# Performance work log

Hardware: AMD Instinct MI355X
Metric: run time of the kernel (lower is better)

The kernel has to match this reference:

```python
import jax, jax.numpy as jnp
import numpy as np

BN_EPS = 1e-4  # matches torch.nn.BatchNorm1d(eps=0.0001)

def setup_inputs() -> dict:
    key = jax.random.key(0)
    ks = jax.random.split(key, 8)
    N, T, D_in, D_out = 512, 64, 1024, 1024
    return {
        "input_feature_st": jax.random.randint(ks[0], (N, T, D_in), 0, 2).astype(jnp.float32),
        "input_features_sc": jax.random.normal(ks[1], (N, D_in), dtype=jnp.float32),
        "weight": jax.random.normal(ks[2], (D_out, D_in), dtype=jnp.float32) * 0.03,
        "bias": jax.random.normal(ks[3], (D_out,), dtype=jnp.float32) * 0.1,
        "gamma": jax.random.normal(ks[4], (D_out,), dtype=jnp.float32) * 2.0,  # nn.init.normal_(bn.weight, 0, 2.0)
        "beta": jnp.zeros((D_out,), dtype=jnp.float32),
        "running_mean": jax.random.normal(ks[5], (D_out,), dtype=jnp.float32) * 0.1,
        "running_var": jax.random.uniform(ks[6], (D_out,), dtype=jnp.float32, minval=0.5, maxval=1.5),
    }

def _if_scan(pot_in, bias_step):
    # pot_in: (N, T, D_out); bias_step: (D_out,) -> spikes (N, T, D_out)
    pot0 = jnp.zeros(pot_in.shape[::2], dtype=pot_in.dtype)  # (N, D_out)
    def step(pot, p_t):
        pot = pot + p_t + bias_step
        spk = (pot >= 1.0).astype(pot.dtype)
        return pot - spk, spk
    _, spikes_t = jax.lax.scan(step, pot0, jnp.swapaxes(pot_in, 0, 1))  # (T, N, D)
    return jnp.swapaxes(spikes_t, 0, 1)

def reference(input_feature_st, input_features_sc, weight, bias, gamma, beta, running_mean, running_var):
    T = input_feature_st.shape[1]
    # ANN path: Linear + BN (eval stats) + ReLU
    lin = input_features_sc @ weight.T + bias                      # (N, D_out)
    out_bn = gamma * (lin - running_mean) / jnp.sqrt(running_var + BN_EPS) + beta
    ann_output = jax.nn.relu(out_bn)
    # Fold BN into weights for the SNN path (note: no eps, as in source)
    ratio = gamma / jnp.sqrt(running_var)
    w_norm = weight * ratio[:, None]                               # (D_out, D_in)
    b_norm = (bias - running_mean) * ratio + beta                  # (D_out,)
    # Integrate-and-fire scan over T
    pot_in = jnp.einsum("ntd,od->nto", input_feature_st, w_norm)  # (N, T, D_out)
    spike_out = _if_scan(pot_in, b_norm / T)
    spike_count_out = jnp.sum(spike_out, axis=1)                   # (N, D_out)
    return spike_out, spike_count_out
```

## Files before the change

### kernel.cpp

```cpp
#include <hip/hip_runtime.h>
#include <hip/hip_bf16.h>

typedef float  float4v __attribute__((ext_vector_type(4)));
typedef short  short8v __attribute__((ext_vector_type(8)));
typedef short  short4v __attribute__((ext_vector_type(4)));
typedef __bf16 bf16x8  __attribute__((ext_vector_type(8)));
typedef float  f32x4   __attribute__((ext_vector_type(4)));

constexpr int NB = 512, T = 64, DIN = 1024, DOUT = 1024;
constexpr int BM = 128, BN = 128, BK = 64;

constexpr size_t ABF_BYTES = (size_t)NB * T * DIN * 2;
constexpr size_t WN_BYTES  = (size_t)DOUT * DIN * 2;
constexpr size_t WS_BF16   = ABF_BYTES + WN_BYTES;

__device__ __forceinline__ short f2bf_rne(float x) {
    return __builtin_bit_cast(short, __float2bfloat16(x));
}
__device__ __forceinline__ short f2bf_trunc(float x) {
    return (short)(__builtin_bit_cast(unsigned int, x) >> 16);
}
__device__ __forceinline__ void load_lds_16B(const void* g, void* l) {
    __builtin_amdgcn_global_load_lds(
        (const __attribute__((address_space(1))) unsigned int*)g,
        (__attribute__((address_space(3))) unsigned int*)l, 16, 0, 0);
}

__global__ void __launch_bounds__(256)
prep_a_kernel(const float* __restrict__ A, short* __restrict__ Abf) {
    int idx = blockIdx.x * 256 + threadIdx.x;
    const float4v* p = (const float4v*)A + (size_t)idx * 2;
    float4v v0 = __builtin_nontemporal_load(p);
    float4v v1 = __builtin_nontemporal_load(p + 1);
    short8v s;
    #pragma unroll
    for (int j = 0; j < 4; j++) {
        s[j]     = f2bf_trunc(v0[j]);
        s[j + 4] = f2bf_trunc(v1[j]);
    }
    *((short8v*)Abf + idx) = s;
}

__global__ void __launch_bounds__(256)
fold_w_kernel(const float* __restrict__ W, const float* __restrict__ gamma,
              const float* __restrict__ rvar, short* __restrict__ Wn) {
    int idx = blockIdx.x * 256 + threadIdx.x;
    int o = idx >> 8;
    float r = gamma[o] / sqrtf(rvar[o]);
    float4v w = ((const float4v*)W)[idx];
    short4v s;
    #pragma unroll
    for (int j = 0; j < 4; j++) s[j] = f2bf_rne(w[j] * r);
    ((short4v*)Wn)[idx] = s;
}

__global__ void __launch_bounds__(256, 4)
snn_gemm_if_dma(const short* __restrict__ Abf,
                const short* __restrict__ Wn,
                const float* __restrict__ bias, const float* __restrict__ gamma,
                const float* __restrict__ beta, const float* __restrict__ rmean,
                const float* __restrict__ rvar, float* __restrict__ out) {
    __shared__ __align__(16) char smem[32768];
    __shared__ float bstepS[BN];
    char* AsS   = smem;
    char* BsS   = smem + 16384;
    float* potS = (float*)smem;

    const int tid = threadIdx.x;
    const int bs  = blockIdx.x;
    const int oB  = blockIdx.y * BN;

    if (tid < BN) {
        int o = oB + tid;
        float r = gamma[o] / sqrtf(rvar[o]);
        bstepS[tid] = ((bias[o] - rmean[o]) * r + beta[o]) * (1.0f / 64.0f);
    }

    const int lane = tid & 63;
    const int wv   = tid >> 6;
    const int wr   = wv & 1;
    const int wc   = wv >> 1;
    const int l15  = lane & 15;
    const int quad = lane >> 4;

    int srcOff[4];
    #pragma unroll
    for (int i = 0; i < 4; i++) {
        int s   = i * 256 + tid;
        int row = s >> 3;
        int ck  = (s & 7) ^ (row & 7);
        srcOff[i] = (row * DIN + ck * 8) * 2;
    }
    int aOff[4][2], bOff[4][2];
    #pragma unroll
    for (int i = 0; i < 4; i++) {
        int ra = wr * 64 + i * 16 + l15;
        int rb = wc * 64 + i * 16 + l15;
        #pragma unroll
        for (int ks = 0; ks < 2; ks++) {
            int c = ks * 4 + quad;
            aOff[i][ks] = (ra * 8 + (c ^ (ra & 7))) * 16;
            bOff[i][ks] = (rb * 8 + (c ^ (rb & 7))) * 16;
        }
    }

    f32x4 acc[4][4] = {};
    const char* Ab = (const char*)(Abf + (size_t)bs * BM * DIN);
    const char* Bb = (const char*)(Wn + (size_t)oB * DIN);

    for (int kb = 0; kb < DIN; kb += BK) {
        __syncthreads();
        const int kbB = kb * 2;
        #pragma unroll
        for (int i = 0; i < 4; i++) {
            int s = i * 256 + tid;
            load_lds_16B(Ab + srcOff[i] + kbB, AsS + s * 16);
            load_lds_16B(Bb + srcOff[i] + kbB, BsS + s * 16);
        }
        __syncthreads();

        #pragma unroll
        for (int ks = 0; ks < 2; ks++) {
            bf16x8 af[4], bf[4];
            #pragma unroll
            for (int i = 0; i < 4; i++)
                af[i] = __builtin_bit_cast(bf16x8, *(const short8v*)(AsS + aOff[i][ks]));
            #pragma unroll
            for (int i = 0; i < 4; i++)
                bf[i] = __builtin_bit_cast(bf16x8, *(const short8v*)(BsS + bOff[i][ks]));
            #pragma unroll
            for (int mi = 0; mi < 4; mi++)
                #pragma unroll
                for (int ni = 0; ni < 4; ni++)
                    acc[mi][ni] = __builtin_amdgcn_mfma_f32_16x16x32_bf16(
                        af[mi], bf[ni], acc[mi][ni], 0, 0, 0);
        }
    }

    __syncthreads();

    #pragma unroll 1
    for (int s = 0; s < 2; s++) {
        if (wr == s) {
            #pragma unroll
            for (int mi = 0; mi < 4; mi++)
                #pragma unroll
                for (int ni = 0; ni < 4; ni++)
                    #pragma unroll
                    for (int r = 0; r < 4; r++) {
                        int row = mi * 16 + quad * 4 + r;
                        int col = (wc * 64 + ni * 16 + l15) ^ (quad << 3);
                        potS[row * BN + col] = acc[mi][ni][r];
                    }
        }
        __syncthreads();
        if (tid < BN) {
            int n = bs * 2 + s;
            float pot = 0.f, cnt = 0.f;
            const float bst = bstepS[tid];
            float* so = out + (size_t)n * T * DOUT + oB + tid;
            for (int t = 0; t < T; t++) {
                pot += potS[t * BN + (tid ^ (((t >> 2) & 3) << 3))] + bst;
                float spk = (pot >= 1.0f) ? 1.0f : 0.0f;
                pot -= spk;
                cnt += spk;
                __builtin_nontemporal_store(spk, so + (size_t)t * DOUT);
            }
            __builtin_nontemporal_store(
                cnt, out + (size_t)NB * T * DOUT + (size_t)n * DOUT + oB + tid);
        }
        __syncthreads();
    }
}


constexpr int LDA_F = 72;
constexpr int A_BYTES_F = BM * LDA_F * 2;
constexpr int SMEM_F = A_BYTES_F + BN * BK * 2;

template <bool PREFOLD>
__global__ void __launch_bounds__(256)
snn_gemm_if(const float* __restrict__ A, const float* __restrict__ W,
            const short* __restrict__ Wn,
            const float* __restrict__ bias, const float* __restrict__ gamma,
            const float* __restrict__ beta, const float* __restrict__ rmean,
            const float* __restrict__ rvar, float* __restrict__ out) {
    __shared__ __align__(16) char smem[SMEM_F];
    __shared__ float ratioS[BN];
    __shared__ float bstepS[BN];
    short* AsS  = (short*)smem;
    short* BsS  = (short*)(smem + A_BYTES_F);
    float* potS = (float*)smem;

    const int tid   = threadIdx.x;
    const int by    = blockIdx.y;
    const int oBase = blockIdx.x * BN;

    if (tid < BN) {
        int o = oBase + tid;
        float r = gamma[o] / sqrtf(rvar[o]);
        ratioS[tid] = r;
        bstepS[tid] = ((bias[o] - rmean[o]) * r + beta[o]) * (1.0f / 64.0f);
    }
    __syncthreads();

    const int lane = tid & 63;
    const int wv   = tid >> 6;
    const int wr   = wv & 1;
    const int wc   = wv >> 1;
    const int l15  = lane & 15;
    const int quad = lane >> 4;

    f32x4 acc[4][4] = {};
    const float* Ab = A + (size_t)by * BM * DIN;

    for (int kb = 0; kb < DIN; kb += BK) {
        float4v av[4][2];
        #pragma unroll
        for (int i = 0; i < 4; i++) {
            int g = i * 256 + tid;
            int r = g >> 3, k8 = g & 7;
            const float4v* p = (const float4v*)(Ab + (size_t)r * DIN + kb + k8 * 8);
            av[i][0] = p[0];
            av[i][1] = p[1];
        }
        float4v bv[4][2];
        if constexpr (!PREFOLD) {
            #pragma unroll
            for (int i = 0; i < 4; i++) {
                int slot = i * 256 + tid;
                int r = slot >> 3, k8 = (slot & 7) ^ (r & 7);
                const float4v* p = (const float4v*)(W + (size_t)(oBase + r) * DIN + kb + k8 * 8);
                bv[i][0] = p[0];
                bv[i][1] = p[1];
            }
        }
        __syncthreads();

        if constexpr (PREFOLD) {
            #pragma unroll
            for (int i = 0; i < 4; i++) {
                int slot = i * 256 + tid;
                int r = slot >> 3, k8 = (slot & 7) ^ (r & 7);
                load_lds_16B(Wn + (size_t)(oBase + r) * DIN + kb + k8 * 8,
                             BsS + (size_t)slot * 8);
            }
        } else {
            #pragma unroll
            for (int i = 0; i < 4; i++) {
                int slot = i * 256 + tid;
                int r = slot >> 3;
                float rt = ratioS[r];
                short8v s;
                #pragma unroll
                for (int j = 0; j < 4; j++) {
                    s[j]     = f2bf_rne(bv[i][0][j] * rt);
                    s[j + 4] = f2bf_rne(bv[i][1][j] * rt);
                }
                *(short8v*)(BsS + (size_t)slot * 8) = s;
            }
        }
        #pragma unroll
        for (int i = 0; i < 4; i++) {
            int g = i * 256 + tid;
            int r = g >> 3, k8 = g & 7;
            short8v s;
            #pragma unroll
            for (int j = 0; j < 4; j++) {
                s[j]     = f2bf_trunc(av[i][0][j]);
                s[j + 4] = f2bf_trunc(av[i][1][j]);
            }
            *(short8v*)(&AsS[r * LDA_F + k8 * 8]) = s;
        }
        __syncthreads();

        #pragma unroll
        for (int ks = 0; ks < 2; ks++) {
            bf16x8 af[4], bfv[4];
            #pragma unroll
            for (int mi = 0; mi < 4; mi++)
                af[mi] = __builtin_bit_cast(bf16x8,
                    *(const short8v*)(&AsS[(wr * 64 + mi * 16 + l15) * LDA_F + ks * 32 + quad * 8]));
            #pragma unroll
            for (int ni = 0; ni < 4; ni++) {
                int row  = wc * 64 + ni * 16 + l15;
                int slot = row * 8 + ((ks * 4 + quad) ^ (l15 & 7));
                bfv[ni] = __builtin_bit_cast(bf16x8, *(const short8v*)(BsS + (size_t)slot * 8));
            }
            #pragma unroll
            for (int mi = 0; mi < 4; mi++)
                #pragma unroll
                for (int ni = 0; ni < 4; ni++)
                    acc[mi][ni] = __builtin_amdgcn_mfma_f32_16x16x32_bf16(
                        af[mi], bfv[ni], acc[mi][ni], 0, 0, 0);
        }
    }

    __syncthreads();

    #pragma unroll 1
    for (int s = 0; s < 2; s++) {
        if (wr == s) {
            #pragma unroll
            for (int mi = 0; mi < 4; mi++)
                #pragma unroll
                for (int ni = 0; ni < 4; ni++)
                    #pragma unroll
                    for (int r = 0; r < 4; r++)
                        potS[(mi * 16 + quad * 4 + r) * BN + wc * 64 + ni * 16 + l15] =
                            acc[mi][ni][r];
        }
        __syncthreads();
        if (tid < BN) {
            int n = by * 2 + s;
            float pot = 0.f, cnt = 0.f;
            const float bst = bstepS[tid];
            float* so = out + (size_t)n * T * DOUT + oBase + tid;
            for (int t = 0; t < T; t++) {
                pot += potS[t * BN + tid] + bst;
                float spk = (pot >= 1.0f) ? 1.0f : 0.0f;
                pot -= spk;
                cnt += spk;
                so[(size_t)t * DOUT] = spk;
            }
            out[(size_t)NB * T * DOUT + (size_t)n * DOUT + oBase + tid] = cnt;
        }
        __syncthreads();
    }
}

extern "C" void kernel_launch(void* const* d_in, const int* in_sizes, int n_in,
                              void* d_out, int out_size, void* d_ws, size_t ws_size,
                              hipStream_t stream) {
    const float* A     = (const float*)d_in[0];
    const float* W     = (const float*)d_in[2];
    const float* bias  = (const float*)d_in[3];
    const float* gamma = (const float*)d_in[4];
    const float* beta  = (const float*)d_in[5];
    const float* rmean = (const float*)d_in[6];
    const float* rvar  = (const float*)d_in[7];
    float* out = (float*)d_out;

    if (d_ws != nullptr && ws_size >= WS_BF16) {
        short* Abf = (short*)d_ws;
        short* Wn  = (short*)((char*)d_ws + ABF_BYTES);
        prep_a_kernel<<<(NB * T * DIN) / 8 / 256, 256, 0, stream>>>(A, Abf);
        fold_w_kernel<<<DOUT * DIN / 4 / 256, 256, 0, stream>>>(W, gamma, rvar, Wn);
        dim3 grid(NB / 2, DOUT / BN);
        snn_gemm_if_dma<<<grid, 256, 0, stream>>>(Abf, Wn, bias, gamma, beta,
                                                  rmean, rvar, out);
    } else if (d_ws != nullptr && ws_size >= WN_BYTES) {
        short* Wn = (short*)d_ws;
        fold_w_kernel<<<DOUT * DIN / 4 / 256, 256, 0, stream>>>(W, gamma, rvar, Wn);
        dim3 grid(DOUT / BN, NB / 2);
        snn_gemm_if<true><<<grid, 256, 0, stream>>>(A, W, Wn, bias, gamma, beta,
                                                    rmean, rvar, out);
    } else {
        dim3 grid(DOUT / BN, NB / 2);
        snn_gemm_if<false><<<grid, 256, 0, stream>>>(A, W, nullptr, bias, gamma, beta,
                                                     rmean, rvar, out);
    }
}
```

Measured before the change: 305.3 us.

## Use 256x256 tiles with triple-buffered async LDS pipeline and fused prep kernel

Replaces the 128x128 single-buffered bf16 GEMM with a 512-thread 256x256 tile kernel. It uses BK=32, three LDS buffers loaded by direct global-to-LDS DMA, and waits on vmcnt so loads overlap MFMA compute, with priority raised around the MFMA block. The two prep kernels for A conversion and W folding are merged into one launch. The larger tiles reduce global reloads of A and W, but the grid shrinks to 512 blocks, more LDS is used per block, and the scan epilogue now covers 4 batch rows per block.

```diff
diff --git a/kernel.cpp b/kernel.cpp
--- a/kernel.cpp
+++ b/kernel.cpp
@@ -8,7 +8,6 @@
 typedef float  f32x4   __attribute__((ext_vector_type(4)));
 
 constexpr int NB = 512, T = 64, DIN = 1024, DOUT = 1024;
-constexpr int BM = 128, BN = 128, BK = 64;
 
 constexpr size_t ABF_BYTES = (size_t)NB * T * DIN * 2;
 constexpr size_t WN_BYTES  = (size_t)DOUT * DIN * 2;
@@ -26,19 +25,36 @@
         (__attribute__((address_space(3))) unsigned int*)l, 16, 0, 0);
 }
 
+constexpr int PREP_A_BLOCKS = NB * T * DIN / 8 / 256;
+constexpr int PREP_W_BLOCKS = DOUT * DIN / 4 / 256;
+
 __global__ void __launch_bounds__(256)
-prep_a_kernel(const float* __restrict__ A, short* __restrict__ Abf) {
-    int idx = blockIdx.x * 256 + threadIdx.x;
-    const float4v* p = (const float4v*)A + (size_t)idx * 2;
-    float4v v0 = __builtin_nontemporal_load(p);
-    float4v v1 = __builtin_nontemporal_load(p + 1);
-    short8v s;
-    #pragma unroll
-    for (int j = 0; j < 4; j++) {
-        s[j]     = f2bf_trunc(v0[j]);
-        s[j + 4] = f2bf_trunc(v1[j]);
-    }
-    *((short8v*)Abf + idx) = s;
+prep_fused(const float* __restrict__ A, short* __restrict__ Abf,
+           const float* __restrict__ W, const float* __restrict__ gamma,
+           const float* __restrict__ rvar, short* __restrict__ Wn) {
+    const int b = blockIdx.x;
+    if (b < PREP_A_BLOCKS) {
+        int idx = b * 256 + threadIdx.x;
+        const float4v* p = (const float4v*)A + (size_t)idx * 2;
+        float4v v0 = __builtin_nontemporal_load(p);
+        float4v v1 = __builtin_nontemporal_load(p + 1);
+        short8v s;
+        #pragma unroll
+        for (int j = 0; j < 4; j++) {
+            s[j]     = f2bf_trunc(v0[j]);
+            s[j + 4] = f2bf_trunc(v1[j]);
+        }
+        *((short8v*)Abf + idx) = s;
+    } else {
+        int idx = (b - PREP_A_BLOCKS) * 256 + threadIdx.x;
+        int o = idx >> 8;
+        float r = gamma[o] / sqrtf(rvar[o]);
+        float4v w = ((const float4v*)W)[idx];
+        short4v s;
+        #pragma unroll
+        for (int j = 0; j < 4; j++) s[j] = f2bf_rne(w[j] * r);
+        ((short4v*)Wn)[idx] = s;
+    }
 }
 
 __global__ void __launch_bounds__(256)
@@ -54,23 +70,25 @@
     ((short4v*)Wn)[idx] = s;
 }
 
-__global__ void __launch_bounds__(256, 4)
-snn_gemm_if_dma(const short* __restrict__ Abf,
+constexpr int BM2 = 256, BN2 = 256, BK2 = 32;
+constexpr int NSTEP2 = DIN / BK2;
+constexpr int BUFB   = (BM2 + BN2) * BK2 * 2;
+constexpr int BREG   = BM2 * BK2 * 2;
+
+__global__ void __launch_bounds__(512, 2)
+snn_gemm_if_256(const short* __restrict__ Abf,
                 const short* __restrict__ Wn,
                 const float* __restrict__ bias, const float* __restrict__ gamma,
                 const float* __restrict__ beta, const float* __restrict__ rmean,
                 const float* __restrict__ rvar, float* __restrict__ out) {
-    __shared__ __align__(16) char smem[32768];
-    __shared__ float bstepS[BN];
-    char* AsS   = smem;
-    char* BsS   = smem + 16384;
-    float* potS = (float*)smem;
+    __shared__ __align__(16) char sm[3 * BUFB];
+    __shared__ float bstepS[BN2];
 
     const int tid = threadIdx.x;
-    const int bs  = blockIdx.x;
-    const int oB  = blockIdx.y * BN;
-
-    if (tid < BN) {
+    const int oB  = blockIdx.x * BN2;
+    const int bs  = blockIdx.y;
+
+    if (tid < BN2) {
         int o = oB + tid;
         float r = gamma[o] / sqrtf(rvar[o]);
         bstepS[tid] = ((bias[o] - rmean[o]) * r + beta[o]) * (1.0f / 64.0f);
@@ -78,89 +96,114 @@
 
     const int lane = tid & 63;
     const int wv   = tid >> 6;
-    const int wr   = wv & 1;
-    const int wc   = wv >> 1;
+    const int wr   = wv >> 2;
+    const int wc   = wv & 3;
     const int l15  = lane & 15;
     const int quad = lane >> 4;
 
-    int srcOff[4];
+    int aOff[8], bOff[4];
     #pragma unroll
-    for (int i = 0; i < 4; i++) {
-        int s   = i * 256 + tid;
-        int row = s >> 3;
-        int ck  = (s & 7) ^ (row & 7);
-        srcOff[i] = (row * DIN + ck * 8) * 2;
-    }
-    int aOff[4][2], bOff[4][2];
+    for (int mi = 0; mi < 8; mi++) {
+        int r = wr * 128 + mi * 16 + l15;
+        aOff[mi] = (r * 4 + (quad ^ ((r >> 1) & 3))) * 16;
+    }
     #pragma unroll
-    for (int i = 0; i < 4; i++) {
-        int ra = wr * 64 + i * 16 + l15;
-        int rb = wc * 64 + i * 16 + l15;
-        #pragma unroll
-        for (int ks = 0; ks < 2; ks++) {
-            int c = ks * 4 + quad;
-            aOff[i][ks] = (ra * 8 + (c ^ (ra & 7))) * 16;
-            bOff[i][ks] = (rb * 8 + (c ^ (rb & 7))) * 16;
-        }
-    }
-
-    f32x4 acc[4][4] = {};
-    const char* Ab = (const char*)(Abf + (size_t)bs * BM * DIN);
-    const char* Bb = (const char*)(Wn + (size_t)oB * DIN);
-
-    for (int kb = 0; kb < DIN; kb += BK) {
-        __syncthreads();
-        const int kbB = kb * 2;
-        #pragma unroll
-        for (int i = 0; i < 4; i++) {
-            int s = i * 256 + tid;
-            load_lds_16B(Ab + srcOff[i] + kbB, AsS + s * 16);
-            load_lds_16B(Bb + srcOff[i] + kbB, BsS + s * 16);
-        }
-        __syncthreads();
-
-        #pragma unroll
-        for (int ks = 0; ks < 2; ks++) {
-            bf16x8 af[4], bf[4];
-            #pragma unroll
-            for (int i = 0; i < 4; i++)
-                af[i] = __builtin_bit_cast(bf16x8, *(const short8v*)(AsS + aOff[i][ks]));
-            #pragma unroll
-            for (int i = 0; i < 4; i++)
-                bf[i] = __builtin_bit_cast(bf16x8, *(const short8v*)(BsS + bOff[i][ks]));
-            #pragma unroll
-            for (int mi = 0; mi < 4; mi++)
+    for (int ni = 0; ni < 4; ni++) {
+        int r = wc * 64 + ni * 16 + l15;
+        bOff[ni] = BREG + (r * 4 + (quad ^ ((r >> 1) & 3))) * 16;
+    }
+
+    f32x4 acc[8][4] = {};
+
+    const int s0 = tid, s1 = 512 + tid;
+    const int r0 = s0 >> 2, r1 = s1 >> 2;
+    const int c0 = (s0 & 3) ^ ((r0 >> 1) & 3);
+    const int c1 = (s1 & 3) ^ ((r1 >> 1) & 3);
+    const short* gA0 = Abf + (size_t)(bs * BM2 + r0) * DIN + c0 * 8;
+    const short* gA1 = Abf + (size_t)(bs * BM2 + r1) * DIN + c1 * 8;
+    const short* gB0 = Wn + (size_t)(oB + r0) * DIN + c0 * 8;
+    const short* gB1 = Wn + (size_t)(oB + r1) * DIN + c1 * 8;
+    const int dA0 = s0 * 16, dA1 = s1 * 16;
+    const int dB0 = BREG + s0 * 16, dB1 = BREG + s1 * 16;
+
+    auto STAGE = [&](int bufB) {
+        load_lds_16B(gA0, sm + bufB + dA0);
+        load_lds_16B(gA1, sm + bufB + dA1);
+        load_lds_16B(gB0, sm + bufB + dB0);
+        load_lds_16B(gB1, sm + bufB + dB1);
+        gA0 += BK2; gA1 += BK2; gB0 += BK2; gB1 += BK2;
+    };
+    auto COMPUTE = [&](int bufB) {
+        const char* base = sm + bufB;
+        bf16x8 af[8], bv[4];
+        #pragma unroll
+        for (int mi = 0; mi < 8; mi++)
+            af[mi] = __builtin_bit_cast(bf16x8, *(const short8v*)(base + aOff[mi]));
+        #pragma unroll
+        for (int ni = 0; ni < 4; ni++)
+            bv[ni] = __builtin_bit_cast(bf16x8, *(const short8v*)(base + bOff[ni]));
+        __builtin_amdgcn_s_setprio(1);
+        #pragma unroll
+        for (int mi = 0; mi < 8; mi++)
+            #pragma unroll
+            for (int ni = 0; ni < 4; ni++)
+                acc[mi][ni] = __builtin_amdgcn_mfma_f32_16x16x32_bf16(
+                    af[mi], bv[ni], acc[mi][ni], 0, 0, 0);
+        __builtin_amdgcn_s_setprio(0);
+    };
+
+    STAGE(0);
+    STAGE(BUFB);
+    asm volatile("s_waitcnt vmcnt(4)" ::: "memory");
+    __builtin_amdgcn_sched_barrier(0);
+    __builtin_amdgcn_s_barrier();
+    __builtin_amdgcn_sched_barrier(0);
+
+    int cb = 0, sb = 2 * BUFB;
+    #pragma unroll 1
+    for (int t = 0; t < NSTEP2 - 2; ++t) {
+        STAGE(sb);
+        COMPUTE(cb);
+        asm volatile("s_waitcnt vmcnt(4)" ::: "memory");
+        __builtin_amdgcn_sched_barrier(0);
+        __builtin_amdgcn_s_barrier();
+        __builtin_amdgcn_sched_barrier(0);
+        cb = (cb == 2 * BUFB) ? 0 : cb + BUFB;
+        sb = (sb == 2 * BUFB) ? 0 : sb + BUFB;
+    }
+    COMPUTE(0);
+    asm volatile("s_waitcnt vmcnt(0)" ::: "memory");
+    __builtin_amdgcn_sched_barrier(0);
+    __builtin_amdgcn_s_barrier();
+    __builtin_amdgcn_sched_barrier(0);
+    COMPUTE(BUFB);
+
+    __syncthreads();
+
+    float* potS = (float*)sm;
+    #pragma unroll
+    for (int s = 0; s < 4; ++s) {
+        if (wr == (s >> 1)) {
+            const int mib = (s & 1) * 4;
+            #pragma unroll
+            for (int m2 = 0; m2 < 4; ++m2)
                 #pragma unroll
-                for (int ni = 0; ni < 4; ni++)
-                    acc[mi][ni] = __builtin_amdgcn_mfma_f32_16x16x32_bf16(
-                        af[mi], bf[ni], acc[mi][ni], 0, 0, 0);
-        }
-    }
-
-    __syncthreads();
-
-    #pragma unroll 1
-    for (int s = 0; s < 2; s++) {
-        if (wr == s) {
-            #pragma unroll
-            for (int mi = 0; mi < 4; mi++)
-                #pragma unroll
-                for (int ni = 0; ni < 4; ni++)
+                for (int ni = 0; ni < 4; ++ni)
                     #pragma unroll
-                    for (int r = 0; r < 4; r++) {
-                        int row = mi * 16 + quad * 4 + r;
+                    for (int r = 0; r < 4; ++r) {
+                        int rl  = m2 * 16 + quad * 4 + r;
                         int col = (wc * 64 + ni * 16 + l15) ^ (quad << 3);
-                        potS[row * BN + col] = acc[mi][ni][r];
+                        potS[rl * BN2 + col] = acc[mib + m2][ni][r];
                     }
         }
         __syncthreads();
-        if (tid < BN) {
-            int n = bs * 2 + s;
+        if (tid < BN2) {
+            int n = bs * 4 + s;
             float pot = 0.f, cnt = 0.f;
             const float bst = bstepS[tid];
             float* so = out + (size_t)n * T * DOUT + oB + tid;
             for (int t = 0; t < T; t++) {
-                pot += potS[t * BN + (tid ^ (((t >> 2) & 3) << 3))] + bst;
+                pot += potS[t * BN2 + (tid ^ (((t >> 2) & 3) << 3))] + bst;
                 float spk = (pot >= 1.0f) ? 1.0f : 0.0f;
                 pot -= spk;
                 cnt += spk;
@@ -174,6 +217,7 @@
 }
 
 
+constexpr int BM = 128, BN = 128, BK = 64;
 constexpr int LDA_F = 72;
 constexpr int A_BYTES_F = BM * LDA_F * 2;
 constexpr int SMEM_F = A_BYTES_F + BN * BK * 2;
@@ -344,10 +388,10 @@
     if (d_ws != nullptr && ws_size >= WS_BF16) {
         short* Abf = (short*)d_ws;
         short* Wn  = (short*)((char*)d_ws + ABF_BYTES);
-        prep_a_kernel<<<(NB * T * DIN) / 8 / 256, 256, 0, stream>>>(A, Abf);
-        fold_w_kernel<<<DOUT * DIN / 4 / 256, 256, 0, stream>>>(W, gamma, rvar, Wn);
-        dim3 grid(NB / 2, DOUT / BN);
-        snn_gemm_if_dma<<<grid, 256, 0, stream>>>(Abf, Wn, bias, gamma, beta,
+        prep_fused<<<PREP_A_BLOCKS + PREP_W_BLOCKS, 256, 0, stream>>>(
+            A, Abf, W, gamma, rvar, Wn);
+        dim3 grid(DOUT / BN2, NB / 4);
+        snn_gemm_if_256<<<grid, 512, 0, stream>>>(Abf, Wn, bias, gamma, beta,
                                                   rmean, rvar, out);
     } else if (d_ws != nullptr && ws_size >= WN_BYTES) {
         short* Wn = (short*)d_ws;
```

Result: slower. 320.7 us (+5.0%).

## Double-buffer A tiles in LDS, load B fragments directly to registers, remap grid

Applied to the files above, without the earlier changes.

Restructures the GEMM main loop so A tiles are double-buffered in LDS via async global-to-LDS loads, which leaves one barrier per K step instead of two. B (the folded weights) is read straight from global memory into registers instead of being staged through LDS. The 1D grid is remapped so the 8 output-column tiles of the same row panel spread across XCDs, and the two prep kernels are fused into a single launch. The trade-off is more global traffic for B, which should mostly hit cache, plus higher register pressure, and launch bounds drop to 3 blocks per CU.

```diff
diff --git a/kernel.cpp b/kernel.cpp
--- a/kernel.cpp
+++ b/kernel.cpp
@@ -8,7 +8,6 @@
 typedef float  f32x4   __attribute__((ext_vector_type(4)));
 
 constexpr int NB = 512, T = 64, DIN = 1024, DOUT = 1024;
-constexpr int BM = 128, BN = 128, BK = 64;
 
 constexpr size_t ABF_BYTES = (size_t)NB * T * DIN * 2;
 constexpr size_t WN_BYTES  = (size_t)DOUT * DIN * 2;
@@ -26,19 +25,36 @@
         (__attribute__((address_space(3))) unsigned int*)l, 16, 0, 0);
 }
 
+constexpr int PREP_A_BLOCKS = NB * T * DIN / 8 / 256;
+constexpr int PREP_W_BLOCKS = DOUT * DIN / 4 / 256;
+
 __global__ void __launch_bounds__(256)
-prep_a_kernel(const float* __restrict__ A, short* __restrict__ Abf) {
-    int idx = blockIdx.x * 256 + threadIdx.x;
-    const float4v* p = (const float4v*)A + (size_t)idx * 2;
-    float4v v0 = __builtin_nontemporal_load(p);
-    float4v v1 = __builtin_nontemporal_load(p + 1);
-    short8v s;
-    #pragma unroll
-    for (int j = 0; j < 4; j++) {
-        s[j]     = f2bf_trunc(v0[j]);
-        s[j + 4] = f2bf_trunc(v1[j]);
-    }
-    *((short8v*)Abf + idx) = s;
+prep_fused(const float* __restrict__ A, short* __restrict__ Abf,
+           const float* __restrict__ W, const float* __restrict__ gamma,
+           const float* __restrict__ rvar, short* __restrict__ Wn) {
+    const int b = blockIdx.x;
+    if (b < PREP_A_BLOCKS) {
+        int idx = b * 256 + threadIdx.x;
+        const float4v* p = (const float4v*)A + (size_t)idx * 2;
+        float4v v0 = __builtin_nontemporal_load(p);
+        float4v v1 = __builtin_nontemporal_load(p + 1);
+        short8v s;
+        #pragma unroll
+        for (int j = 0; j < 4; j++) {
+            s[j]     = f2bf_trunc(v0[j]);
+            s[j + 4] = f2bf_trunc(v1[j]);
+        }
+        *((short8v*)Abf + idx) = s;
+    } else {
+        int idx = (b - PREP_A_BLOCKS) * 256 + threadIdx.x;
+        int o = idx >> 8;
+        float r = gamma[o] / sqrtf(rvar[o]);
+        float4v w = ((const float4v*)W)[idx];
+        short4v s;
+        #pragma unroll
+        for (int j = 0; j < 4; j++) s[j] = f2bf_rne(w[j] * r);
+        ((short4v*)Wn)[idx] = s;
+    }
 }
 
 __global__ void __launch_bounds__(256)
@@ -54,21 +70,24 @@
     ((short4v*)Wn)[idx] = s;
 }
 
-__global__ void __launch_bounds__(256, 4)
-snn_gemm_if_dma(const short* __restrict__ Abf,
-                const short* __restrict__ Wn,
-                const float* __restrict__ bias, const float* __restrict__ gamma,
-                const float* __restrict__ beta, const float* __restrict__ rmean,
-                const float* __restrict__ rvar, float* __restrict__ out) {
-    __shared__ __align__(16) char smem[32768];
+constexpr int BM = 128, BN = 128, BK = 64;
+constexpr int NT = DIN / BK;
+constexpr int ABUF = BM * BK * 2;
+
+__global__ void __launch_bounds__(256, 3)
+snn_gemm_if_breg(const short* __restrict__ Abf,
+                 const short* __restrict__ Wn,
+                 const float* __restrict__ bias, const float* __restrict__ gamma,
+                 const float* __restrict__ beta, const float* __restrict__ rmean,
+                 const float* __restrict__ rvar, float* __restrict__ out) {
+    __shared__ __align__(16) char sm[2 * ABUF];
     __shared__ float bstepS[BN];
-    char* AsS   = smem;
-    char* BsS   = smem + 16384;
-    float* potS = (float*)smem;
 
     const int tid = threadIdx.x;
-    const int bs  = blockIdx.x;
-    const int oB  = blockIdx.y * BN;
+    const int b     = blockIdx.x;
+    const int work  = (b & 7) * 256 + (b >> 3);
+    const int panel = work >> 3;
+    const int oB    = (work & 7) * BN;
 
     if (tid < BN) {
         int o = oB + tid;
@@ -91,54 +110,68 @@
         int ck  = (s & 7) ^ (row & 7);
         srcOff[i] = (row * DIN + ck * 8) * 2;
     }
-    int aOff[4][2], bOff[4][2];
+    int aOff[4][2];
     #pragma unroll
     for (int i = 0; i < 4; i++) {
         int ra = wr * 64 + i * 16 + l15;
-        int rb = wc * 64 + i * 16 + l15;
         #pragma unroll
         for (int ks = 0; ks < 2; ks++) {
             int c = ks * 4 + quad;
             aOff[i][ks] = (ra * 8 + (c ^ (ra & 7))) * 16;
-            bOff[i][ks] = (rb * 8 + (c ^ (rb & 7))) * 16;
-        }
-    }
+        }
+    }
+
+    const short* gBf[4];
+    #pragma unroll
+    for (int ni = 0; ni < 4; ni++)
+        gBf[ni] = Wn + (size_t)(oB + wc * 64 + ni * 16 + l15) * DIN + quad * 8;
 
     f32x4 acc[4][4] = {};
-    const char* Ab = (const char*)(Abf + (size_t)bs * BM * DIN);
-    const char* Bb = (const char*)(Wn + (size_t)oB * DIN);
-
-    for (int kb = 0; kb < DIN; kb += BK) {
-        __syncthreads();
-        const int kbB = kb * 2;
-        #pragma unroll
-        for (int i = 0; i < 4; i++) {
-            int s = i * 256 + tid;
-            load_lds_16B(Ab + srcOff[i] + kbB, AsS + s * 16);
-            load_lds_16B(Bb + srcOff[i] + kbB, BsS + s * 16);
-        }
-        __syncthreads();
-
+    const char* Ab = (const char*)(Abf + (size_t)panel * BM * DIN);
+    char* As0 = sm;
+    char* As1 = sm + ABUF;
+
+    #pragma unroll
+    for (int i = 0; i < 4; i++)
+        load_lds_16B(Ab + srcOff[i], As0 + (i * 256 + tid) * 16);
+    __syncthreads();
+
+    #pragma unroll 1
+    for (int t = 0; t < NT; ++t) {
+        const int kb = t * BK;
+        short8v bvr[4][2];
+        #pragma unroll
+        for (int ni = 0; ni < 4; ni++)
+            #pragma unroll
+            for (int ks = 0; ks < 2; ks++)
+                bvr[ni][ks] = *(const short8v*)(gBf[ni] + kb + ks * 32);
+        __builtin_amdgcn_sched_barrier(0);
+        if (t < NT - 1) {
+            const int kbB = (kb + BK) * 2;
+            #pragma unroll
+            for (int i = 0; i < 4; i++)
+                load_lds_16B(Ab + srcOff[i] + kbB, As1 + (i * 256 + tid) * 16);
+        }
         #pragma unroll
         for (int ks = 0; ks < 2; ks++) {
-            bf16x8 af[4], bf[4];
+            bf16x8 af[4];
             #pragma unroll
             for (int i = 0; i < 4; i++)
-                af[i] = __builtin_bit_cast(bf16x8, *(const short8v*)(AsS + aOff[i][ks]));
-            #pragma unroll
-            for (int i = 0; i < 4; i++)
-                bf[i] = __builtin_bit_cast(bf16x8, *(const short8v*)(BsS + bOff[i][ks]));
+                af[i] = __builtin_bit_cast(bf16x8,
+                    *(const short8v*)(As0 + aOff[i][ks]));
             #pragma unroll
             for (int mi = 0; mi < 4; mi++)
                 #pragma unroll
                 for (int ni = 0; ni < 4; ni++)
                     acc[mi][ni] = __builtin_amdgcn_mfma_f32_16x16x32_bf16(
-                        af[mi], bf[ni], acc[mi][ni], 0, 0, 0);
-        }
-    }
-
-    __syncthreads();
-
+                        af[mi], __builtin_bit_cast(bf16x8, bvr[ni][ks]),
+                        acc[mi][ni], 0, 0, 0);
+        }
+        __syncthreads();
+        char* tmp = As0; As0 = As1; As1 = tmp;
+    }
+
+    float* potS = (float*)sm;
     #pragma unroll 1
     for (int s = 0; s < 2; s++) {
         if (wr == s) {
@@ -155,7 +188,7 @@
         }
         __syncthreads();
         if (tid < BN) {
-            int n = bs * 2 + s;
+            int n = panel * 2 + s;
             float pot = 0.f, cnt = 0.f;
             const float bst = bstepS[tid];
             float* so = out + (size_t)n * T * DOUT + oB + tid;
@@ -344,11 +377,10 @@
     if (d_ws != nullptr && ws_size >= WS_BF16) {
         short* Abf = (short*)d_ws;
         short* Wn  = (short*)((char*)d_ws + ABF_BYTES);
-        prep_a_kernel<<<(NB * T * DIN) / 8 / 256, 256, 0, stream>>>(A, Abf);
-        fold_w_kernel<<<DOUT * DIN / 4 / 256, 256, 0, stream>>>(W, gamma, rvar, Wn);
-        dim3 grid(NB / 2, DOUT / BN);
-        snn_gemm_if_dma<<<grid, 256, 0, stream>>>(Abf, Wn, bias, gamma, beta,
-                                                  rmean, rvar, out);
+        prep_fused<<<PREP_A_BLOCKS + PREP_W_BLOCKS, 256, 0, stream>>>(
+            A, Abf, W, gamma, rvar, Wn);
+        snn_gemm_if_breg<<<dim3(2048), 256, 0, stream>>>(Abf, Wn, bias, gamma,
+                                                         beta, rmean, rvar, out);
     } else if (d_ws != nullptr && ws_size >= WN_BYTES) {
         short* Wn = (short*)d_ws;
         fold_w_kernel<<<DOUT * DIN / 4 / 256, 256, 0, stream>>>(W, gamma, rvar, Wn);
```

Result: slower. 367.6 us (+20.4%).
